# Optimization experiments

Hardware: AMD Instinct MI355X
Metric: run time of the kernel (lower is better)

The kernel has to match this reference:

```python
import jax, jax.numpy as jnp
import numpy as np

B, S, E, L = 4, 4096, 64, 3
INIT_SCALE = 0.03


def setup_inputs() -> dict:
    key = jax.random.key(0)
    ks = jax.random.split(key, 7)
    return {
        "x": jax.random.normal(ks[0], (B, S, S + 1), dtype=jnp.float32),
        "q_ws": jax.random.normal(ks[1], (L, E, E), dtype=jnp.float32) * INIT_SCALE,
        "k_ws": jax.random.normal(ks[2], (L, E, E), dtype=jnp.float32) * INIT_SCALE,
        "v_ws": jax.random.normal(ks[3], (L, E, E), dtype=jnp.float32) * INIT_SCALE,
        "random_matrix": jax.random.normal(ks[4], (S, E - 1), dtype=jnp.float32) * INIT_SCALE,
        "coeffs_attended": jax.random.normal(ks[5], (S, E), dtype=jnp.float32) * INIT_SCALE,
        "offset": jax.random.normal(ks[6], (1,), dtype=jnp.float32),
    }


def reference(x, q_ws, k_ws, v_ws, random_matrix, coeffs_attended, offset):
    seq_length = random_matrix.shape[0]
    # project first seq_length feature columns, keep the last column raw -> [B, S, E]
    av = jnp.concatenate(
        [jnp.einsum('bsf,fe->bse', x[:, :, :seq_length], random_matrix), x[:, :, -1:]],
        axis=2,
    )

    def layer(av, ws):
        qw, kw, vw = ws
        q = jnp.einsum('bse,ed->bsd', av, qw)   # [B, S, E]
        k = jnp.einsum('bse,ed->bsd', av, kw)
        v = jnp.einsum('bse,ed->bsd', av, vw)
        scores = jax.nn.softmax(jnp.einsum('bqd,bkd->bqk', q, k), axis=-1)  # [B, S, S]
        out = jnp.einsum('bqk,bkd->bqd', scores, v)
        # skip_connections=False: output replaces attended values
        return out, None

    av, _ = jax.lax.scan(layer, av, (q_ws, k_ws, v_ws))
    final = jnp.einsum('bij,ij->b', av, coeffs_attended)  # [B]
    return final + offset[0]
```

## Files before the change

kernel.cpp:

```cpp
#include <hip/hip_runtime.h>

#define SEQ  4096
#define EMB  64
#define NB   4
#define XROW 4097

#define SW(r, c) ((r) * 64 + (((c) ^ ((r) & 7)) << 3))

typedef unsigned short ushort_t;
typedef __attribute__((ext_vector_type(8))) short short8;
typedef __attribute__((ext_vector_type(4))) float floatx4;

union U8 { uint4 u; short8 s8; };

__device__ __forceinline__ ushort_t f2bf(float f) {
    union { float f; unsigned int u; } v; v.f = f;
    unsigned int r = v.u + 0x7FFFu + ((v.u >> 16) & 1u);
    return (ushort_t)(r >> 16);
}
__device__ __forceinline__ uint2 pack4bf(float a, float b, float c, float d) {
    uint2 p;
    p.x = (unsigned)f2bf(a) | ((unsigned)f2bf(b) << 16);
    p.y = (unsigned)f2bf(c) | ((unsigned)f2bf(d) << 16);
    return p;
}

__global__ __launch_bounds__(256) void prep_rmt(const float* __restrict__ rm,
                                                ushort_t* __restrict__ rmT,
                                                float* __restrict__ out,
                                                const float* __restrict__ offset) {
    if (blockIdx.x == 0 && threadIdx.x < NB) out[threadIdx.x] = offset[0];
    int o = (blockIdx.x * 256 + threadIdx.x) * 4;
    int e = o >> 12;
    int f = o & 4095;
    alignas(8) ushort_t t[4];
    t[0] = f2bf((e < 63) ? rm[(size_t)(f + 0) * 63 + e] : 0.f);
    t[1] = f2bf((e < 63) ? rm[(size_t)(f + 1) * 63 + e] : 0.f);
    t[2] = f2bf((e < 63) ? rm[(size_t)(f + 2) * 63 + e] : 0.f);
    t[3] = f2bf((e < 63) ? rm[(size_t)(f + 3) * 63 + e] : 0.f);
    *(uint2*)&rmT[o] = *(uint2*)t;
}

__global__ __launch_bounds__(512) void proj_mfma(const float* __restrict__ x,
        const ushort_t* __restrict__ rmT, float* __restrict__ av) {
    __shared__ ushort_t xs[2][64 * 64];
    __shared__ ushort_t rs[2][64 * 64];
    const int tid = threadIdx.x;
    const int row0 = blockIdx.x * 64;
    const int w = tid >> 6, l = tid & 63;
    const int wg = w >> 2;
    const int wq = w & 3;
    const int t4 = tid & 255;
    const int srow = t4 >> 2, sc = (t4 & 3) * 16;
    const int c0 = (t4 & 3) * 2;
    const int kbase = wg * 2048;
    const int quad = l >> 4, q16 = l & 15;

    floatx4 acc[4];
    #pragma unroll
    for (int i = 0; i < 4; ++i) acc[i] = (floatx4){0.f, 0.f, 0.f, 0.f};

    float px[16];
    short8 pr0, pr1;
    {
        const float* xp = x + (size_t)(row0 + srow) * XROW + kbase + sc;
        #pragma unroll
        for (int i = 0; i < 16; ++i) px[i] = xp[i];
        const ushort_t* rp = rmT + (size_t)srow * SEQ + kbase + sc;
        pr0 = *(const short8*)&rp[0];
        pr1 = *(const short8*)&rp[8];
    }

    for (int k0 = 0; k0 < 2048; k0 += 64) {
        __syncthreads();
        {
            alignas(16) ushort_t tmp[16];
            #pragma unroll
            for (int i = 0; i < 16; ++i) tmp[i] = f2bf(px[i]);
            *(short8*)&xs[wg][SW(srow, c0)]     = *(short8*)&tmp[0];
            *(short8*)&xs[wg][SW(srow, c0 + 1)] = *(short8*)&tmp[8];
            *(short8*)&rs[wg][SW(srow, c0)]     = pr0;
            *(short8*)&rs[wg][SW(srow, c0 + 1)] = pr1;
        }
        __syncthreads();
        if (k0 + 64 < 2048) {
            const float* xp = x + (size_t)(row0 + srow) * XROW + kbase + k0 + 64 + sc;
            #pragma unroll
            for (int i = 0; i < 16; ++i) px[i] = xp[i];
            const ushort_t* rp = rmT + (size_t)srow * SEQ + kbase + k0 + 64 + sc;
            pr0 = *(const short8*)&rp[0];
            pr1 = *(const short8*)&rp[8];
        }
        #pragma unroll
        for (int ksp = 0; ksp < 2; ++ksp) {
            short8 a = *(short8*)&xs[wg][SW(wq * 16 + q16, ksp * 4 + quad)];
            #pragma unroll
            for (int nt = 0; nt < 4; ++nt) {
                short8 bf = *(short8*)&rs[wg][SW(nt * 16 + q16, ksp * 4 + quad)];
                acc[nt] = __builtin_amdgcn_mfma_f32_16x16x32_bf16(a, bf, acc[nt], 0, 0, 0);
            }
        }
    }

    __syncthreads();
    float* poc = (float*)xs;
    if (wg == 1) {
        #pragma unroll
        for (int nt = 0; nt < 4; ++nt)
            #pragma unroll
            for (int r = 0; r < 4; ++r)
                poc[(wq * 16 + quad * 4 + r) * 64 + nt * 16 + q16] = acc[nt][r];
    }
    __syncthreads();
    if (wg == 0) {
        #pragma unroll
        for (int nt = 0; nt < 4; ++nt)
            #pragma unroll
            for (int r = 0; r < 4; ++r) {
                int row = row0 + wq * 16 + quad * 4 + r;
                int col = nt * 16 + q16;
                float v = acc[nt][r] + poc[(wq * 16 + quad * 4 + r) * 64 + col];
                if (col == 63) v = x[(size_t)row * XROW + SEQ];
                av[(size_t)row * EMB + col] = v;
            }
    }
}

__global__ __launch_bounds__(256) void qkv_mfma(const float* __restrict__ av,
        const float* __restrict__ qw, const float* __restrict__ kw,
        const float* __restrict__ vw, ushort_t* __restrict__ Qb,
        ushort_t* __restrict__ Kb, ushort_t* __restrict__ Vt) {
    __shared__ ushort_t avs[64 * 64];
    __shared__ ushort_t wqs[64 * 64], wks[64 * 64], wvs[64 * 64];
    const int tid = threadIdx.x;
    const int row0 = blockIdx.x * 64;
    const int w = tid >> 6, l = tid & 63;
    const int srow = tid >> 2, sc = (tid & 3) * 16;
    const int c0 = (tid & 3) * 2;

    {
        const float* ap = av + (size_t)(row0 + srow) * EMB + sc;
        alignas(16) ushort_t tmp[16];
        #pragma unroll
        for (int i = 0; i < 16; ++i) tmp[i] = f2bf(ap[i]);
        *(short8*)&avs[SW(srow, c0)]     = *(short8*)&tmp[0];
        *(short8*)&avs[SW(srow, c0 + 1)] = *(short8*)&tmp[8];
    }
    {
        alignas(16) ushort_t tq[16], tk[16], tv[16];
        #pragma unroll
        for (int i = 0; i < 16; ++i) {
            int kk = sc + i;
            tq[i] = f2bf(qw[kk * 64 + srow]);
            tk[i] = f2bf(kw[kk * 64 + srow]);
            tv[i] = f2bf(vw[kk * 64 + srow]);
        }
        *(short8*)&wqs[SW(srow, c0)]     = *(short8*)&tq[0];
        *(short8*)&wqs[SW(srow, c0 + 1)] = *(short8*)&tq[8];
        *(short8*)&wks[SW(srow, c0)]     = *(short8*)&tk[0];
        *(short8*)&wks[SW(srow, c0 + 1)] = *(short8*)&tk[8];
        *(short8*)&wvs[SW(srow, c0)]     = *(short8*)&tv[0];
        *(short8*)&wvs[SW(srow, c0 + 1)] = *(short8*)&tv[8];
    }
    __syncthreads();

    floatx4 aq[4], ak[4], avv[4];
    #pragma unroll
    for (int i = 0; i < 4; ++i) {
        aq[i] = (floatx4){0.f, 0.f, 0.f, 0.f};
        ak[i] = aq[i]; avv[i] = aq[i];
    }
    #pragma unroll
    for (int ksp = 0; ksp < 2; ++ksp) {
        short8 a = *(short8*)&avs[SW(w * 16 + (l & 15), ksp * 4 + (l >> 4))];
        #pragma unroll
        for (int nt = 0; nt < 4; ++nt) {
            int bo = SW(nt * 16 + (l & 15), ksp * 4 + (l >> 4));
            aq[nt]  = __builtin_amdgcn_mfma_f32_16x16x32_bf16(a, *(short8*)&wqs[bo], aq[nt], 0, 0, 0);
            ak[nt]  = __builtin_amdgcn_mfma_f32_16x16x32_bf16(a, *(short8*)&wks[bo], ak[nt], 0, 0, 0);
            avv[nt] = __builtin_amdgcn_mfma_f32_16x16x32_bf16(a, *(short8*)&wvs[bo], avv[nt], 0, 0, 0);
        }
    }

    const int b = row0 >> 12;
    #pragma unroll
    for (int nt = 0; nt < 4; ++nt)
        #pragma unroll
        for (int r = 0; r < 4; ++r) {
            int row = row0 + w * 16 + (l >> 4) * 4 + r;
            int col = nt * 16 + (l & 15);
            size_t o = (size_t)row * EMB + col;
            Qb[o] = f2bf(aq[nt][r]);
            Kb[o] = f2bf(ak[nt][r]);
            Vt[((size_t)b * EMB + col) * SEQ + (row & 4095)] = f2bf(avv[nt][r]);
        }
}

__global__ __launch_bounds__(512) void flash_mfma(const ushort_t* __restrict__ Qb,
        const ushort_t* __restrict__ Kb, const ushort_t* __restrict__ Vt,
        float* __restrict__ out) {
    __shared__ ushort_t psbuf[8 * 2048];
    __shared__ float comb[3][64 * 64];
    __shared__ float lrow[4][64];
    const int tid = threadIdx.x;
    const int w = tid >> 6, l = tid & 63;
    const int wg = w >> 1;
    const int wq = w & 1;
    const int quad = l >> 4, q16 = l & 15;
    const int id2 = (blockIdx.x & 7) * 32 + (blockIdx.x >> 3);
    const int b = id2 >> 6;
    const int q0 = (id2 & 63) * 64;
    const size_t base  = (size_t)b * SEQ * EMB;
    const size_t vbase = (size_t)b * EMB * SEQ;
    const int kbase = wg * 1024;
    ushort_t* ps = &psbuf[w * 2048];

    short8 qf[2][2];
    #pragma unroll
    for (int qh = 0; qh < 2; ++qh)
        #pragma unroll
        for (int ksp = 0; ksp < 2; ++ksp)
            qf[qh][ksp] = *(const short8*)&Qb[base
                + (size_t)(q0 + wq * 32 + qh * 16 + q16) * EMB + ksp * 32 + quad * 8];

    floatx4 o_acc[2][4];
    #pragma unroll
    for (int qh = 0; qh < 2; ++qh)
        #pragma unroll
        for (int i = 0; i < 4; ++i) o_acc[qh][i] = (floatx4){0.f, 0.f, 0.f, 0.f};
    float lp0 = 0.f, lp1 = 0.f;

    for (int kt0 = 0; kt0 < 1024; kt0 += 64) {
        const int kt = kbase + kt0;

        floatx4 s[2][4];
        #pragma unroll
        for (int qh = 0; qh < 2; ++qh)
            #pragma unroll
            for (int nt = 0; nt < 4; ++nt) s[qh][nt] = (floatx4){0.f, 0.f, 0.f, 0.f};
        #pragma unroll
        for (int ksp = 0; ksp < 2; ++ksp) {
            short8 akf[4];
            #pragma unroll
            for (int nt = 0; nt < 4; ++nt)
                akf[nt] = *(const short8*)&Kb[base
                    + (size_t)(kt + nt * 16 + q16) * EMB + ksp * 32 + quad * 8];
            #pragma unroll
            for (int nt = 0; nt < 4; ++nt) {
                s[0][nt] = __builtin_amdgcn_mfma_f32_16x16x32_bf16(akf[nt], qf[0][ksp], s[0][nt], 0, 0, 0);
                s[1][nt] = __builtin_amdgcn_mfma_f32_16x16x32_bf16(akf[nt], qf[1][ksp], s[1][nt], 0, 0, 0);
            }
        }

        short8 bv[2][4];
        #pragma unroll
        for (int ksp = 0; ksp < 2; ++ksp)
            #pragma unroll
            for (int nt = 0; nt < 4; ++nt)
                bv[ksp][nt] = *(const short8*)&Vt[vbase
                    + (size_t)(nt * 16 + q16) * SEQ + kt + ksp * 32 + quad * 8];

        #pragma unroll
        for (int nt = 0; nt < 4; ++nt) {
            float p0 = __expf(s[0][nt][0]);
            float p1 = __expf(s[0][nt][1]);
            float p2 = __expf(s[0][nt][2]);
            float p3 = __expf(s[0][nt][3]);
            lp0 += (p0 + p1) + (p2 + p3);
            int g = nt * 4 + quad;
            *(uint2*)&ps[q16 * 64 + ((g ^ q16) & 15) * 4] = pack4bf(p0, p1, p2, p3);
        }
        #pragma unroll
        for (int nt = 0; nt < 4; ++nt) {
            float p0 = __expf(s[1][nt][0]);
            float p1 = __expf(s[1][nt][1]);
            float p2 = __expf(s[1][nt][2]);
            float p3 = __expf(s[1][nt][3]);
            lp1 += (p0 + p1) + (p2 + p3);
            int g = nt * 4 + quad;
            *(uint2*)&ps[1024 + q16 * 64 + ((g ^ q16) & 15) * 4] = pack4bf(p0, p1, p2, p3);
        }
        asm volatile("s_waitcnt lgkmcnt(0)" ::: "memory");

        #pragma unroll
        for (int ksp = 0; ksp < 2; ++ksp) {
            #pragma unroll
            for (int qh = 0; qh < 2; ++qh) {
                int g0 = ksp * 8 + quad * 2;
                uint2 a0 = *(uint2*)&ps[qh * 1024 + q16 * 64 + ((g0 ^ q16) & 15) * 4];
                uint2 a1 = *(uint2*)&ps[qh * 1024 + q16 * 64 + (((g0 + 1) ^ q16) & 15) * 4];
                U8 af;
                af.u.x = a0.x; af.u.y = a0.y; af.u.z = a1.x; af.u.w = a1.y;
                #pragma unroll
                for (int nt = 0; nt < 4; ++nt)
                    o_acc[qh][nt] = __builtin_amdgcn_mfma_f32_16x16x32_bf16(af.s8, bv[ksp][nt], o_acc[qh][nt], 0, 0, 0);
            }
        }
    }

    lp0 += __shfl_xor(lp0, 16);
    lp0 += __shfl_xor(lp0, 32);
    lp1 += __shfl_xor(lp1, 16);
    lp1 += __shfl_xor(lp1, 32);
    if (quad == 0) {
        lrow[wg][wq * 32 + q16]      = lp0;
        lrow[wg][wq * 32 + 16 + q16] = lp1;
    }
    if (wg > 0) {
        #pragma unroll
        for (int qh = 0; qh < 2; ++qh)
            #pragma unroll
            for (int nt = 0; nt < 4; ++nt)
                #pragma unroll
                for (int r = 0; r < 4; ++r)
                    comb[wg - 1][(wq * 32 + qh * 16 + quad * 4 + r) * 64 + nt * 16 + q16]
                        = o_acc[qh][nt][r];
    }
    __syncthreads();
    if (wg == 0) {
        #pragma unroll
        for (int qh = 0; qh < 2; ++qh) {
            float linv[4];
            #pragma unroll
            for (int r = 0; r < 4; ++r) {
                int ql = wq * 32 + qh * 16 + quad * 4 + r;
                linv[r] = 1.f / (lrow[0][ql] + lrow[1][ql] + lrow[2][ql] + lrow[3][ql]);
            }
            #pragma unroll
            for (int nt = 0; nt < 4; ++nt)
                #pragma unroll
                for (int r = 0; r < 4; ++r) {
                    int ql = wq * 32 + qh * 16 + quad * 4 + r;
                    int col = nt * 16 + q16;
                    float v = (o_acc[qh][nt][r] + comb[0][ql * 64 + col]
                               + comb[1][ql * 64 + col] + comb[2][ql * 64 + col]) * linv[r];
                    out[base + (size_t)(q0 + ql) * EMB + col] = v;
                }
        }
    }
}

__global__ __launch_bounds__(256) void reduce_kernel(const float* __restrict__ av,
        const float* __restrict__ coeffs, float* __restrict__ out) {
    const int b = blockIdx.y;
    const size_t base = (size_t)b * SEQ * EMB;
    const int local0 = blockIdx.x * 4096;
    const int tid = threadIdx.x;
    float ssum = 0.f;
    #pragma unroll
    for (int i = 0; i < 4; ++i) {
        int idx = local0 + (tid + i * 256) * 4;
        float4 a = *(const float4*)&av[base + idx];
        float4 c = *(const float4*)&coeffs[idx];
        ssum += a.x * c.x + a.y * c.y + a.z * c.z + a.w * c.w;
    }
    #pragma unroll
    for (int off = 1; off < 64; off <<= 1) ssum += __shfl_xor(ssum, off);
    __shared__ float wsum[4];
    if ((tid & 63) == 0) wsum[tid >> 6] = ssum;
    __syncthreads();
    if (tid == 0)
        atomicAdd(&out[b], wsum[0] + wsum[1] + wsum[2] + wsum[3]);
}

extern "C" void kernel_launch(void* const* d_in, const int* in_sizes, int n_in,
                              void* d_out, int out_size, void* d_ws, size_t ws_size,
                              hipStream_t stream) {
    const float* x      = (const float*)d_in[0];
    const float* q_ws   = (const float*)d_in[1];
    const float* k_ws   = (const float*)d_in[2];
    const float* v_ws   = (const float*)d_in[3];
    const float* rm     = (const float*)d_in[4];
    const float* coeffs = (const float*)d_in[5];
    const float* offset = (const float*)d_in[6];
    float* out = (float*)d_out;
    char* ws = (char*)d_ws;

    float*    AV  = (float*)ws;
    ushort_t* Qb  = (ushort_t*)(ws + 4 * 1024 * 1024);
    ushort_t* Kb  = (ushort_t*)(ws + 6 * 1024 * 1024);
    ushort_t* Vt  = (ushort_t*)(ws + 8 * 1024 * 1024);
    ushort_t* rmT = (ushort_t*)(ws + 10 * 1024 * 1024);

    prep_rmt<<<256, 256, 0, stream>>>(rm, rmT, out, offset);
    proj_mfma<<<256, 512, 0, stream>>>(x, rmT, AV);
    for (int layer = 0; layer < 3; ++layer) {
        qkv_mfma<<<256, 256, 0, stream>>>(AV, q_ws + layer * 4096,
                                          k_ws + layer * 4096, v_ws + layer * 4096,
                                          Qb, Kb, Vt);
        flash_mfma<<<256, 512, 0, stream>>>(Qb, Kb, Vt, AV);
    }
    reduce_kernel<<<dim3(64, NB), 256, 0, stream>>>(AV, coeffs, out);
}
```

Before: 593.8 us.

## Stage K and V tiles through shared memory with register prefetch in flash kernel

Each block now cooperatively loads K and V tiles into swizzled LDS buffers, one per key-quarter, with the next tile prefetched into registers. Previously each wave read K and V directly from global memory, so the two waves sharing a quarter loaded the same data twice. The grid indexing also changes from a remapped 1D index to a 2D (query tile, batch) grid, which drops the earlier block-order swizzle. In exchange the kernel adds two block-wide barriers per iteration and about 64KB more LDS, which may reduce occupancy.

New measurement: 523.3 us. 1.13x faster.

```diff
diff --git a/kernel.cpp b/kernel.cpp
--- a/kernel.cpp
+++ b/kernel.cpp
@@ -199,6 +199,8 @@
 __global__ __launch_bounds__(512) void flash_mfma(const ushort_t* __restrict__ Qb,
         const ushort_t* __restrict__ Kb, const ushort_t* __restrict__ Vt,
         float* __restrict__ out) {
+    __shared__ ushort_t ks[4][64 * 64];
+    __shared__ ushort_t vt[4][64 * 64];
     __shared__ ushort_t psbuf[8 * 2048];
     __shared__ float comb[3][64 * 64];
     __shared__ float lrow[4][64];
@@ -207,11 +209,14 @@
     const int wg = w >> 1;
     const int wq = w & 1;
     const int quad = l >> 4, q16 = l & 15;
-    const int id2 = (blockIdx.x & 7) * 32 + (blockIdx.x >> 3);
-    const int b = id2 >> 6;
-    const int q0 = (id2 & 63) * 64;
+    const int b = blockIdx.y;
+    const int q0 = blockIdx.x * 64;
     const size_t base  = (size_t)b * SEQ * EMB;
     const size_t vbase = (size_t)b * EMB * SEQ;
+    const int qtr  = tid >> 7;
+    const int t7   = tid & 127;
+    const int srow = t7 >> 1;
+    const int hc   = (t7 & 1) * 4;
     const int kbase = wg * 1024;
     ushort_t* ps = &psbuf[w * 2048];
 
@@ -223,6 +228,17 @@
             qf[qh][ksp] = *(const short8*)&Qb[base
                 + (size_t)(q0 + wq * 32 + qh * 16 + q16) * EMB + ksp * 32 + quad * 8];
 
+    short8 pk[4], pv[4];
+    {
+        const ushort_t* kp = Kb + base + (size_t)(qtr * 1024 + srow) * EMB + hc * 8;
+        const ushort_t* vp = Vt + vbase + (size_t)srow * SEQ + qtr * 1024 + hc * 8;
+        #pragma unroll
+        for (int j = 0; j < 4; ++j) {
+            pk[j] = *(const short8*)(kp + j * 8);
+            pv[j] = *(const short8*)(vp + j * 8);
+        }
+    }
+
     floatx4 o_acc[2][4];
     #pragma unroll
     for (int qh = 0; qh < 2; ++qh)
@@ -231,7 +247,22 @@
     float lp0 = 0.f, lp1 = 0.f;
 
     for (int kt0 = 0; kt0 < 1024; kt0 += 64) {
-        const int kt = kbase + kt0;
+        __syncthreads();
+        #pragma unroll
+        for (int j = 0; j < 4; ++j) {
+            *(short8*)&ks[qtr][SW(srow, hc + j)] = pk[j];
+            *(short8*)&vt[qtr][SW(srow, hc + j)] = pv[j];
+        }
+        __syncthreads();
+        if (kt0 + 64 < 1024) {
+            const ushort_t* kp = Kb + base + (size_t)(qtr * 1024 + kt0 + 64 + srow) * EMB + hc * 8;
+            const ushort_t* vp = Vt + vbase + (size_t)srow * SEQ + qtr * 1024 + kt0 + 64 + hc * 8;
+            #pragma unroll
+            for (int j = 0; j < 4; ++j) {
+                pk[j] = *(const short8*)(kp + j * 8);
+                pv[j] = *(const short8*)(vp + j * 8);
+            }
+        }
 
         floatx4 s[2][4];
         #pragma unroll
@@ -240,25 +271,13 @@
             for (int nt = 0; nt < 4; ++nt) s[qh][nt] = (floatx4){0.f, 0.f, 0.f, 0.f};
         #pragma unroll
         for (int ksp = 0; ksp < 2; ++ksp) {
-            short8 akf[4];
-            #pragma unroll
-            for (int nt = 0; nt < 4; ++nt)
-                akf[nt] = *(const short8*)&Kb[base
-                    + (size_t)(kt + nt * 16 + q16) * EMB + ksp * 32 + quad * 8];
             #pragma unroll
             for (int nt = 0; nt < 4; ++nt) {
-                s[0][nt] = __builtin_amdgcn_mfma_f32_16x16x32_bf16(akf[nt], qf[0][ksp], s[0][nt], 0, 0, 0);
-                s[1][nt] = __builtin_amdgcn_mfma_f32_16x16x32_bf16(akf[nt], qf[1][ksp], s[1][nt], 0, 0, 0);
-            }
-        }
-
-        short8 bv[2][4];
-        #pragma unroll
-        for (int ksp = 0; ksp < 2; ++ksp)
-            #pragma unroll
-            for (int nt = 0; nt < 4; ++nt)
-                bv[ksp][nt] = *(const short8*)&Vt[vbase
-                    + (size_t)(nt * 16 + q16) * SEQ + kt + ksp * 32 + quad * 8];
+                short8 a = *(short8*)&ks[wg][SW(nt * 16 + q16, ksp * 4 + quad)];
+                s[0][nt] = __builtin_amdgcn_mfma_f32_16x16x32_bf16(a, qf[0][ksp], s[0][nt], 0, 0, 0);
+                s[1][nt] = __builtin_amdgcn_mfma_f32_16x16x32_bf16(a, qf[1][ksp], s[1][nt], 0, 0, 0);
+            }
+        }
 
         #pragma unroll
         for (int nt = 0; nt < 4; ++nt) {
@@ -284,6 +303,10 @@
 
         #pragma unroll
         for (int ksp = 0; ksp < 2; ++ksp) {
+            short8 bv[4];
+            #pragma unroll
+            for (int nt = 0; nt < 4; ++nt)
+                bv[nt] = *(short8*)&vt[wg][SW(nt * 16 + q16, ksp * 4 + quad)];
             #pragma unroll
             for (int qh = 0; qh < 2; ++qh) {
                 int g0 = ksp * 8 + quad * 2;
@@ -293,7 +316,7 @@
                 af.u.x = a0.x; af.u.y = a0.y; af.u.z = a1.x; af.u.w = a1.y;
                 #pragma unroll
                 for (int nt = 0; nt < 4; ++nt)
-                    o_acc[qh][nt] = __builtin_amdgcn_mfma_f32_16x16x32_bf16(af.s8, bv[ksp][nt], o_acc[qh][nt], 0, 0, 0);
+                    o_acc[qh][nt] = __builtin_amdgcn_mfma_f32_16x16x32_bf16(af.s8, bv[nt], o_acc[qh][nt], 0, 0, 0);
             }
         }
     }
@@ -388,7 +411,7 @@
         qkv_mfma<<<256, 256, 0, stream>>>(AV, q_ws + layer * 4096,
                                           k_ws + layer * 4096, v_ws + layer * 4096,
                                           Qb, Kb, Vt);
-        flash_mfma<<<256, 512, 0, stream>>>(Qb, Kb, Vt, AV);
+        flash_mfma<<<dim3(64, NB), 512, 0, stream>>>(Qb, Kb, Vt, AV);
     }
     reduce_kernel<<<dim3(64, NB), 256, 0, stream>>>(AV, coeffs, out);
 }
```
